# Kernel optimization log

Hardware: AMD Instinct MI355X
Metric: run time of the kernel (lower is better)

## Reference

```python
import jax, jax.numpy as jnp
import numpy as np

N = 50000
E = 800000
IN_C, HID_C, OUT_C = 256, 128, 64


def setup_inputs() -> dict:
    key = jax.random.key(0)
    k1, k2, k3, k4 = jax.random.split(key, 4)
    x = jax.random.normal(k1, (N, IN_C), dtype=jnp.float32)
    edge_index = jax.random.randint(k2, (2, E), 0, N, dtype=jnp.int64)
    # Glorot-ish init for GCN weights, zero bias (PyG default)
    W1 = jax.random.normal(k3, (IN_C, HID_C), dtype=jnp.float32) / np.sqrt(IN_C)
    b1 = jnp.zeros((HID_C,), dtype=jnp.float32)
    W2 = jax.random.normal(k4, (HID_C, OUT_C), dtype=jnp.float32) / np.sqrt(HID_C)
    b2 = jnp.zeros((OUT_C,), dtype=jnp.float32)
    return {"x": x, "edge_index": edge_index, "W1": W1, "b1": b1, "W2": W2, "b2": b2}


def _gcn_norm(edge_index, num_nodes):
    # Add self-loops, compute symmetric normalization D^-1/2 A D^-1/2 (PyG GCNConv default)
    loops = jnp.arange(num_nodes, dtype=edge_index.dtype)
    src = jnp.concatenate([edge_index[0], loops])  # message sources
    dst = jnp.concatenate([edge_index[1], loops])  # aggregation targets
    deg = jax.ops.segment_sum(jnp.ones_like(dst, dtype=jnp.float32), dst,
                              num_segments=num_nodes)
    dinv = jnp.where(deg > 0, jax.lax.rsqrt(deg), 0.0)
    norm = dinv[src] * dinv[dst]  # [E+N]
    return src, dst, norm


def _gcn_conv(x, W, b, src, dst, norm, num_nodes):
    h = x @ W                                   # [N, out]
    msg = h[src] * norm[:, None]                # gather + scale, [E+N, out]
    out = jax.ops.segment_sum(msg, dst, num_segments=num_nodes)  # scatter-add
    return out + b


def reference(x, edge_index, W1, b1, W2, b2):
    num_nodes = x.shape[0]
    src, dst, norm = _gcn_norm(edge_index, num_nodes)
    h = _gcn_conv(x, W1, b1, src, dst, norm, num_nodes)
    h = jax.nn.relu(h)
    # F.dropout(training=False) -> identity at inference
    return _gcn_conv(h, W2, b2, src, dst, norm, num_nodes)
```

## Files before the change

### kernel.cpp

```cpp
#include <hip/hip_runtime.h>
#include <hip/hip_bf16.h>


typedef __attribute__((ext_vector_type(8))) short short8;
typedef __attribute__((ext_vector_type(4))) float f32x4;

union BF8 {
    short8 s;
    uint4 u;
    __hip_bfloat162 h[4];
};

__device__ __forceinline__ unsigned short f32_to_bf16_rne(float f) {
    unsigned u = __float_as_uint(f);
    return (unsigned short)((u + 0x7fffu + ((u >> 16) & 1u)) >> 16);
}
__device__ __forceinline__ float bf_lo(unsigned v) { return __uint_as_float(v << 16); }
__device__ __forceinline__ float bf_hi(unsigned v) { return __uint_as_float(v & 0xffff0000u); }

#define ACHUNK 2048
#define BSH 6
#define BN 64
#define CAP 2048
#define EPT (CAP / 256)

__global__ void wfrag_zero_kernel(const float* __restrict__ W1, const float* __restrict__ W2,
                                  unsigned short* __restrict__ w1f,
                                  unsigned short* __restrict__ w2f,
                                  int* __restrict__ counts, int* __restrict__ bcursor,
                                  int n, int nbk) {
    int i = blockIdx.x * blockDim.x + threadIdx.x;
    if (i < n) counts[i] = 0;
    if (i < nbk) bcursor[i] = 0;
    const float* W;
    unsigned short* WF;
    int KS, NCOL, idx;
    if (i < 32768) {
        W = W1; WF = w1f; KS = 8; NCOL = 128; idx = i;
    } else if (i < 32768 + 8192) {
        W = W2; WF = w2f; KS = 4; NCOL = 64; idx = i - 32768;
    } else return;
    int j = idx & 7;
    int lane = (idx >> 3) & 63;
    int f = idx >> 9;
    int ks = f % KS, nt = f / KS;
    int m16 = lane & 15, quad = lane >> 4;
    int ncol = nt * 16 + m16;
    int k = ks * 32 + quad * 8 + j;
    WF[idx] = f32_to_bf16_rne(W[k * NCOL + ncol]);
}

__global__ __launch_bounds__(256, 8) void gemm1_bucket_kernel(
    const float* __restrict__ A, const unsigned short* __restrict__ BFRAG,
    unsigned short* __restrict__ C, int M, int nbA,
    const int* __restrict__ src, const int* __restrict__ dst,
    int* __restrict__ counts, int* __restrict__ bcursor,
    int2* __restrict__ tmp, int e, int nbk) {
    constexpr int NT = 8, KS = 8;
    constexpr int K = KS * 32;
    constexpr int LSTRIDE = 136;
    __shared__ unsigned short Alds[64 * LSTRIDE];

    const int tid = threadIdx.x;
    if ((int)blockIdx.x >= nbA) {
        const int wave = tid >> 6, lane = tid & 63;
        const int quad = lane >> 4, m16 = lane & 15;
        const int rowBase = (blockIdx.x - nbA) * 64;
        const uint4* Bfrag = (const uint4*)BFRAG + lane;

        f32x4 acc[NT];
#pragma unroll
        for (int nt = 0; nt < NT; nt++) acc[nt] = f32x4{0.f, 0.f, 0.f, 0.f};

#pragma unroll
        for (int h = 0; h < 2; h++) {
            if (h) __syncthreads();
#pragma unroll
            for (int bt = 0; bt < 2; bt++) {
                f32x4 v[4];
#pragma unroll
                for (int it = 0; it < 4; it++) {
                    int p = (bt * 4 + it) * 1024 + tid * 4;
                    int r = p >> 7, c = p & 127;
                    int rg = rowBase + r;
                    if (rg >= M) rg = M - 1;
                    v[it] = *(const f32x4*)(A + (size_t)rg * K + h * 128 + c);
                }
#pragma unroll
                for (int it = 0; it < 4; it++) {
                    int p = (bt * 4 + it) * 1024 + tid * 4;
                    int r = p >> 7, c = p & 127;
                    BF8 cv;
                    cv.h[0] = __float22bfloat162_rn(make_float2(v[it].x, v[it].y));
                    cv.h[1] = __float22bfloat162_rn(make_float2(v[it].z, v[it].w));
                    *(uint2*)&Alds[r * LSTRIDE + c] = make_uint2(cv.u.x, cv.u.y);
                }
            }
            __syncthreads();
            const unsigned short* Afrag0 = &Alds[(wave * 16 + m16) * LSTRIDE + quad * 8];
#pragma unroll
            for (int ks = 0; ks < 4; ks++) {
                BF8 af;
                af.u = *(const uint4*)(Afrag0 + ks * 32);
                int kg = h * 4 + ks;
#pragma unroll
                for (int nt = 0; nt < NT; nt++) {
                    BF8 bf;
                    bf.u = Bfrag[(nt * KS + kg) * 64];
                    acc[nt] = __builtin_amdgcn_mfma_f32_16x16x32_bf16(af.s, bf.s, acc[nt], 0, 0, 0);
                }
            }
        }
        const int rowOut = rowBase + wave * 16 + quad * 4;
#pragma unroll
        for (int nt = 0; nt < NT; nt++) {
#pragma unroll
            for (int r = 0; r < 4; r++) {
                int row = rowOut + r;
                if (row < M)
                    C[(size_t)row * 128 + nt * 16 + m16] = f32_to_bf16_rne(acc[nt][r]);
            }
        }
    } else {
        int* sdst = (int*)Alds;
        int* hist = (int*)((char*)Alds + ACHUNK * 4);
        const int b0 = blockIdx.x;
        const int start = b0 * ACHUNK;
        const int cnt = min(ACHUNK, e - start);
        for (int t = tid; t < nbk; t += 256) hist[t] = 0;
        __syncthreads();
        for (int i = tid; i < cnt; i += 256) {
            int d = dst[start + i];
            sdst[i] = d;
            atomicAdd(&counts[d], 1);
            atomicAdd(&hist[d >> BSH], 1);
        }
        __syncthreads();
        for (int t = tid; t < nbk; t += 256) {
            int h = hist[t];
            hist[t] = (h > 0) ? atomicAdd(&bcursor[t], h) : 0;
        }
        __syncthreads();
        for (int i = tid; i < cnt; i += 256) {
            int d = sdst[i];
            int slot = atomicAdd(&hist[d >> BSH], 1);
            if (slot < CAP)
                tmp[(size_t)(d >> BSH) * CAP + slot] = make_int2(src[start + i], d);
        }
    }
}

__global__ __launch_bounds__(256, 8) void aggsort_gemm2_kernel(
    const int* __restrict__ counts, const int2* __restrict__ tmp,
    const int* __restrict__ bcursor,
    const unsigned short* __restrict__ hb,
    const float* __restrict__ bias1,
    const unsigned short* __restrict__ w2frag,
    int2* __restrict__ sedge, int2* __restrict__ nodeRange,
    unsigned short* __restrict__ h2, int n) {
    constexpr int LSTRIDE = 136;
    __shared__ int ecnt[BN];
    __shared__ int estart[BN];
    __shared__ int lcur[BN];
    __shared__ float ndinv[BN];
    __shared__ unsigned short a1lds[BN * LSTRIDE];

    const int tid = threadIdx.x;
    const int b = blockIdx.x;
    const int nodeBase = b << BSH;
    const int nNodes = min(BN, n - nodeBase);
    const int cnt = min(bcursor[b], CAP);

    if (tid < BN) ecnt[tid] = 0;
    __syncthreads();

    int2 er[EPT];
#pragma unroll
    for (int j = 0; j < EPT; j++) {
        int i = tid + j * 256;
        if (i < cnt) {
            int2 r = tmp[(size_t)b * CAP + i];
            er[j] = r;
            atomicAdd(&ecnt[r.y - nodeBase], 1);
        } else {
            er[j].x = -1;
            er[j].y = 0;
        }
    }
    __syncthreads();

    if (tid < BN) {
        int c = ecnt[tid];
        int x = c;
#pragma unroll
        for (int off = 1; off < 64; off <<= 1) {
            int y = __shfl_up(x, off, 64);
            if (tid >= off) x += y;
        }
        int st = x - c;
        estart[tid] = st;
        lcur[tid] = st;
        ndinv[tid] = rsqrtf((float)c + 1.0f);
        if (tid < nNodes) nodeRange[nodeBase + tid] = make_int2(b * CAP + st, c);
    }
    __syncthreads();

#pragma unroll
    for (int j = 0; j < EPT; j++) {
        if (er[j].x >= 0) {
            int ln = er[j].y - nodeBase;
            float w = rsqrtf((float)counts[er[j].x] + 1.0f) * ndinv[ln];
            int pos = atomicAdd(&lcur[ln], 1);
            sedge[(size_t)b * CAP + pos] = make_int2(er[j].x, __float_as_int(w));
        }
    }
    __syncthreads();

    const int sub = tid & 15;
    const int qw = tid >> 4;
    for (int pass = 0; pass < BN / 16; pass++) {
        int ln = pass * 16 + qw;
        float a0 = 0.f, a1 = 0.f, a2 = 0.f, a3 = 0.f;
        float a4 = 0.f, a5 = 0.f, a6 = 0.f, a7 = 0.f;
        if (ln < nNodes) {
            int node = nodeBase + ln;
            float di = ndinv[ln];
            float d2 = di * di;
            uint4 sv = ((const uint4*)(hb + (size_t)node * 128))[sub];
            a0 = d2 * bf_lo(sv.x); a1 = d2 * bf_hi(sv.x);
            a2 = d2 * bf_lo(sv.y); a3 = d2 * bf_hi(sv.y);
            a4 = d2 * bf_lo(sv.z); a5 = d2 * bf_hi(sv.z);
            a6 = d2 * bf_lo(sv.w); a7 = d2 * bf_hi(sv.w);
            const int2* seg = sedge + (size_t)b * CAP;
            int beg = estart[ln];
            int end = beg + ecnt[ln];
            int i = beg;
            for (; i + 4 <= end; i += 4) {
                int2 e[4]; uint4 v[4];
#pragma unroll
                for (int j = 0; j < 4; j++) e[j] = seg[i + j];
#pragma unroll
                for (int j = 0; j < 4; j++)
                    v[j] = ((const uint4*)(hb + (size_t)e[j].x * 128))[sub];
#pragma unroll
                for (int j = 0; j < 4; j++) {
                    float w = __int_as_float(e[j].y);
                    a0 = fmaf(w, bf_lo(v[j].x), a0); a1 = fmaf(w, bf_hi(v[j].x), a1);
                    a2 = fmaf(w, bf_lo(v[j].y), a2); a3 = fmaf(w, bf_hi(v[j].y), a3);
                    a4 = fmaf(w, bf_lo(v[j].z), a4); a5 = fmaf(w, bf_hi(v[j].z), a5);
                    a6 = fmaf(w, bf_lo(v[j].w), a6); a7 = fmaf(w, bf_hi(v[j].w), a7);
                }
            }
            for (; i < end; ++i) {
                int2 e = seg[i];
                float w = __int_as_float(e.y);
                uint4 v = ((const uint4*)(hb + (size_t)e.x * 128))[sub];
                a0 = fmaf(w, bf_lo(v.x), a0); a1 = fmaf(w, bf_hi(v.x), a1);
                a2 = fmaf(w, bf_lo(v.y), a2); a3 = fmaf(w, bf_hi(v.y), a3);
                a4 = fmaf(w, bf_lo(v.z), a4); a5 = fmaf(w, bf_hi(v.z), a5);
                a6 = fmaf(w, bf_lo(v.w), a6); a7 = fmaf(w, bf_hi(v.w), a7);
            }
            float4 b0v = ((const float4*)bias1)[sub * 2];
            float4 b1v = ((const float4*)bias1)[sub * 2 + 1];
            a0 = fmaxf(a0 + b0v.x, 0.f); a1 = fmaxf(a1 + b0v.y, 0.f);
            a2 = fmaxf(a2 + b0v.z, 0.f); a3 = fmaxf(a3 + b0v.w, 0.f);
            a4 = fmaxf(a4 + b1v.x, 0.f); a5 = fmaxf(a5 + b1v.y, 0.f);
            a6 = fmaxf(a6 + b1v.z, 0.f); a7 = fmaxf(a7 + b1v.w, 0.f);
        }
        BF8 p;
        p.h[0] = __float22bfloat162_rn(make_float2(a0, a1));
        p.h[1] = __float22bfloat162_rn(make_float2(a2, a3));
        p.h[2] = __float22bfloat162_rn(make_float2(a4, a5));
        p.h[3] = __float22bfloat162_rn(make_float2(a6, a7));
        *(uint4*)&a1lds[ln * LSTRIDE + sub * 8] = p.u;
    }
    __syncthreads();

    const int wave = tid >> 6, lane = tid & 63;
    const int quad = lane >> 4, m16 = lane & 15;
    const unsigned short* Afrag0 = &a1lds[(wave * 16 + m16) * LSTRIDE + quad * 8];
    const uint4* Bfrag = (const uint4*)w2frag + lane;

    f32x4 acc[4];
#pragma unroll
    for (int nt = 0; nt < 4; nt++) acc[nt] = f32x4{0.f, 0.f, 0.f, 0.f};
#pragma unroll
    for (int ks = 0; ks < 4; ks++) {
        BF8 af;
        af.u = *(const uint4*)(Afrag0 + ks * 32);
#pragma unroll
        for (int nt = 0; nt < 4; nt++) {
            BF8 bf;
            bf.u = Bfrag[(nt * 4 + ks) * 64];
            acc[nt] = __builtin_amdgcn_mfma_f32_16x16x32_bf16(af.s, bf.s, acc[nt], 0, 0, 0);
        }
    }
    const int rowOut = wave * 16 + quad * 4;
#pragma unroll
    for (int nt = 0; nt < 4; nt++) {
#pragma unroll
        for (int r = 0; r < 4; r++) {
            int row = rowOut + r;
            if (row < nNodes)
                h2[(size_t)(nodeBase + row) * 64 + nt * 16 + m16] =
                    f32_to_bf16_rne(acc[nt][r]);
        }
    }
}

__global__ __launch_bounds__(256, 8) void agg64_kernel(
    const int2* __restrict__ nodeRange, const int2* __restrict__ sedge,
    const unsigned short* __restrict__ hb,
    const float* __restrict__ bias, float* __restrict__ out, int n) {
    int node = blockIdx.x * 16 + (threadIdx.x >> 4);
    if (node >= n) return;
    int sub = threadIdx.x & 15;
    int2 nr = nodeRange[node];
    float di = rsqrtf((float)nr.y + 1.0f);
    float d2 = di * di;
    uint2 sv = ((const uint2*)(hb + (size_t)node * 64))[sub];
    float a0 = d2 * bf_lo(sv.x), a1 = d2 * bf_hi(sv.x);
    float a2 = d2 * bf_lo(sv.y), a3 = d2 * bf_hi(sv.y);
    int beg = nr.x, end = nr.x + nr.y;
    int i = beg;
    for (; i + 8 <= end; i += 8) {
        int2 e[8];
        uint2 v[8];
#pragma unroll
        for (int j = 0; j < 8; j++) e[j] = sedge[i + j];
#pragma unroll
        for (int j = 0; j < 8; j++)
            v[j] = ((const uint2*)(hb + (size_t)e[j].x * 64))[sub];
#pragma unroll
        for (int j = 0; j < 8; j++) {
            float w = __int_as_float(e[j].y);
            a0 = fmaf(w, bf_lo(v[j].x), a0); a1 = fmaf(w, bf_hi(v[j].x), a1);
            a2 = fmaf(w, bf_lo(v[j].y), a2); a3 = fmaf(w, bf_hi(v[j].y), a3);
        }
    }
    for (; i + 4 <= end; i += 4) {
        int2 e[4];
        uint2 v[4];
#pragma unroll
        for (int j = 0; j < 4; j++) e[j] = sedge[i + j];
#pragma unroll
        for (int j = 0; j < 4; j++)
            v[j] = ((const uint2*)(hb + (size_t)e[j].x * 64))[sub];
#pragma unroll
        for (int j = 0; j < 4; j++) {
            float w = __int_as_float(e[j].y);
            a0 = fmaf(w, bf_lo(v[j].x), a0); a1 = fmaf(w, bf_hi(v[j].x), a1);
            a2 = fmaf(w, bf_lo(v[j].y), a2); a3 = fmaf(w, bf_hi(v[j].y), a3);
        }
    }
    for (; i < end; ++i) {
        int2 e = sedge[i];
        float w = __int_as_float(e.y);
        uint2 v = ((const uint2*)(hb + (size_t)e.x * 64))[sub];
        a0 = fmaf(w, bf_lo(v.x), a0); a1 = fmaf(w, bf_hi(v.x), a1);
        a2 = fmaf(w, bf_lo(v.y), a2); a3 = fmaf(w, bf_hi(v.y), a3);
    }
    float4 bv = ((const float4*)bias)[sub];
    ((float4*)(out + (size_t)node * 64))[sub] =
        make_float4(a0 + bv.x, a1 + bv.y, a2 + bv.z, a3 + bv.w);
}

extern "C" void kernel_launch(void* const* d_in, const int* in_sizes, int n_in,
                              void* d_out, int out_size, void* d_ws, size_t ws_size,
                              hipStream_t stream) {
    const float* x  = (const float*)d_in[0];
    const int*   ei = (const int*)d_in[1];
    const float* W1 = (const float*)d_in[2];
    const float* b1 = (const float*)d_in[3];
    const float* W2 = (const float*)d_in[4];
    const float* b2 = (const float*)d_in[5];
    float* out = (float*)d_out;

    const int IN_C = 256;
    const int N = in_sizes[0] / IN_C;
    const int E = in_sizes[1] / 2;
    const int* srcA = ei;
    const int* dstA = ei + E;

    char* ws = (char*)d_ws;
    const size_t KB = 1024, MB = 1024 * 1024;
    int*            counts    = (int*)(ws);
    int*            bcursor   = (int*)(ws + 256 * KB);
    unsigned short* w1f       = (unsigned short*)(ws + 1 * MB);
    unsigned short* w2f       = (unsigned short*)(ws + 1 * MB + 64 * KB);
    int2*           tmp       = (int2*)(ws + 2 * MB);
    int2*           sedge     = (int2*)(ws + 16 * MB);
    int2*           nodeRange = (int2*)(ws + 30 * MB);
    unsigned short* h1b       = (unsigned short*)(ws + 31 * MB);
    unsigned short* h2b       = (unsigned short*)(ws + 44 * MB);

    const int NB = (N + BN - 1) / BN;
    const int gGemm = (N + 63) / 64;
    const int nbA = (E + ACHUNK - 1) / ACHUNK;
    const int gWfrag = (max(N, 32768 + 8192) + 255) / 256;

    wfrag_zero_kernel<<<gWfrag, 256, 0, stream>>>(W1, W2, w1f, w2f, counts, bcursor, N, NB);
    gemm1_bucket_kernel<<<nbA + gGemm, 256, 0, stream>>>(
        x, w1f, h1b, N, nbA, srcA, dstA, counts, bcursor, tmp, E, NB);
    aggsort_gemm2_kernel<<<NB, 256, 0, stream>>>(
        counts, tmp, bcursor, h1b, b1, w2f, sedge, nodeRange, h2b, N);
    agg64_kernel<<<(N + 15) / 16, 256, 0, stream>>>(nodeRange, sedge, h2b, b2, out, N);
}
```

Measured before the change: 242.6 us.

## Replace multi-kernel pipeline with single cooperative persistent kernel using grid syncs

Merges the four launches into one cooperative kernel that uses grid-wide barriers between phases: weight fragment conversion, degree counting, a decoupled-lookback prefix scan fused with GEMM1 tiles, a CSR build through global atomic scatter, then a fused layer-1 aggregation plus GEMM2, and the final aggregation. It drops the bucketed tmp/CAP scheme in favour of an exact rowptr CSR, and shrinks GEMM tiles to 16 rows. The aim is to cut launch gaps and intermediate traffic. In exchange it adds several grid syncs, heavy global atomics on rowptr, serialized lookback spinning, and lower occupancy from the larger persistent kernel.

```diff
diff --git a/kernel.cpp b/kernel.cpp
--- a/kernel.cpp
+++ b/kernel.cpp
@@ -1,5 +1,8 @@
 #include <hip/hip_runtime.h>
 #include <hip/hip_bf16.h>
+#include <hip/hip_cooperative_groups.h>
+
+namespace cg = cooperative_groups;
 
 
 typedef __attribute__((ext_vector_type(8))) short short8;
@@ -18,351 +21,303 @@
 __device__ __forceinline__ float bf_lo(unsigned v) { return __uint_as_float(v << 16); }
 __device__ __forceinline__ float bf_hi(unsigned v) { return __uint_as_float(v & 0xffff0000u); }
 
-#define ACHUNK 2048
-#define BSH 6
-#define BN 64
-#define CAP 2048
-#define EPT (CAP / 256)
-
-__global__ void wfrag_zero_kernel(const float* __restrict__ W1, const float* __restrict__ W2,
-                                  unsigned short* __restrict__ w1f,
-                                  unsigned short* __restrict__ w2f,
-                                  int* __restrict__ counts, int* __restrict__ bcursor,
-                                  int n, int nbk) {
-    int i = blockIdx.x * blockDim.x + threadIdx.x;
-    if (i < n) counts[i] = 0;
-    if (i < nbk) bcursor[i] = 0;
-    const float* W;
-    unsigned short* WF;
-    int KS, NCOL, idx;
-    if (i < 32768) {
-        W = W1; WF = w1f; KS = 8; NCOL = 128; idx = i;
-    } else if (i < 32768 + 8192) {
-        W = W2; WF = w2f; KS = 4; NCOL = 64; idx = i - 32768;
-    } else return;
-    int j = idx & 7;
-    int lane = (idx >> 3) & 63;
-    int f = idx >> 9;
-    int ks = f % KS, nt = f / KS;
-    int m16 = lane & 15, quad = lane >> 4;
-    int ncol = nt * 16 + m16;
-    int k = ks * 32 + quad * 8 + j;
-    WF[idx] = f32_to_bf16_rne(W[k * NCOL + ncol]);
-}
-
-__global__ __launch_bounds__(256, 8) void gemm1_bucket_kernel(
-    const float* __restrict__ A, const unsigned short* __restrict__ BFRAG,
-    unsigned short* __restrict__ C, int M, int nbA,
-    const int* __restrict__ src, const int* __restrict__ dst,
-    int* __restrict__ counts, int* __restrict__ bcursor,
-    int2* __restrict__ tmp, int e, int nbk) {
-    constexpr int NT = 8, KS = 8;
-    constexpr int K = KS * 32;
-    constexpr int LSTRIDE = 136;
-    __shared__ unsigned short Alds[64 * LSTRIDE];
-
+__global__ __launch_bounds__(256) void mega_kernel(
+    const float* __restrict__ x, const int* __restrict__ srcA, const int* __restrict__ dstA,
+    const float* __restrict__ W1, const float* __restrict__ b1,
+    const float* __restrict__ W2, const float* __restrict__ b2,
+    float* __restrict__ out,
+    int* __restrict__ counts, float* __restrict__ dinv, int* __restrict__ rowptr,
+    int* __restrict__ bflag, int* __restrict__ bsum,
+    unsigned short* __restrict__ w1f, unsigned short* __restrict__ w2f,
+    int2* __restrict__ sedge, unsigned short* __restrict__ h1b,
+    unsigned short* __restrict__ h2b,
+    int n, int e, int nScan, int nG1, int nAgg) {
+    cg::grid_group gg = cg::this_grid();
     const int tid = threadIdx.x;
-    if ((int)blockIdx.x >= nbA) {
-        const int wave = tid >> 6, lane = tid & 63;
-        const int quad = lane >> 4, m16 = lane & 15;
-        const int rowBase = (blockIdx.x - nbA) * 64;
-        const uint4* Bfrag = (const uint4*)BFRAG + lane;
-
-        f32x4 acc[NT];
-#pragma unroll
-        for (int nt = 0; nt < NT; nt++) acc[nt] = f32x4{0.f, 0.f, 0.f, 0.f};
-
-#pragma unroll
-        for (int h = 0; h < 2; h++) {
-            if (h) __syncthreads();
-#pragma unroll
-            for (int bt = 0; bt < 2; bt++) {
-                f32x4 v[4];
-#pragma unroll
-                for (int it = 0; it < 4; it++) {
-                    int p = (bt * 4 + it) * 1024 + tid * 4;
-                    int r = p >> 7, c = p & 127;
-                    int rg = rowBase + r;
-                    if (rg >= M) rg = M - 1;
-                    v[it] = *(const f32x4*)(A + (size_t)rg * K + h * 128 + c);
-                }
-#pragma unroll
-                for (int it = 0; it < 4; it++) {
-                    int p = (bt * 4 + it) * 1024 + tid * 4;
-                    int r = p >> 7, c = p & 127;
-                    BF8 cv;
-                    cv.h[0] = __float22bfloat162_rn(make_float2(v[it].x, v[it].y));
-                    cv.h[1] = __float22bfloat162_rn(make_float2(v[it].z, v[it].w));
-                    *(uint2*)&Alds[r * LSTRIDE + c] = make_uint2(cv.u.x, cv.u.y);
-                }
-            }
+    const int bid = blockIdx.x;
+    const int nblk = gridDim.x;
+    const int gstride = nblk * 256;
+    __shared__ char smraw[16 * 136 * 2 + 32];
+
+    {
+        int lim = n > 40960 ? n : 40960;
+        for (int i = bid * 256 + tid; i < lim; i += gstride) {
+            if (i < n) counts[i] = 0;
+            if (i < 64) bflag[i] = 0;
+            if (i < 40960) {
+                const float* W; unsigned short* WF; int KS, NCOL, idx;
+                if (i < 32768) { W = W1; WF = w1f; KS = 8; NCOL = 128; idx = i; }
+                else           { W = W2; WF = w2f; KS = 4; NCOL = 64;  idx = i - 32768; }
+                int j = idx & 7;
+                int lane = (idx >> 3) & 63;
+                int f = idx >> 9;
+                int ks = f % KS, nt = f / KS;
+                int m16 = lane & 15, quad = lane >> 4;
+                WF[idx] = f32_to_bf16_rne(W[(ks * 32 + quad * 8 + j) * NCOL + nt * 16 + m16]);
+            }
+        }
+    }
+    gg.sync();
+
+    for (int i = bid * 256 + tid; i < e; i += gstride)
+        atomicAdd(&counts[dstA[i]], 1);
+    gg.sync();
+
+    for (int it = bid; it < nScan + nG1; it += nblk) {
+        if (it < nScan) {
+            int* wsum = (int*)(smraw + 16 * 136 * 2);
+            const int lane = tid & 63, wv = tid >> 6;
+            int base = it * 1024 + tid * 4;
+            int v[4];
+#pragma unroll
+            for (int j = 0; j < 4; j++) {
+                int i = base + j;
+                if (i < n) {
+                    int c = counts[i];
+                    v[j] = c;
+                    dinv[i] = rsqrtf((float)c + 1.0f);
+                } else v[j] = 0;
+            }
+            int tot = v[0] + v[1] + v[2] + v[3];
+            int xp = tot;
+#pragma unroll
+            for (int off = 1; off < 64; off <<= 1) {
+                int y = __shfl_up(xp, off, 64);
+                if (lane >= off) xp += y;
+            }
+            if (lane == 63) wsum[wv] = xp;
             __syncthreads();
-            const unsigned short* Afrag0 = &Alds[(wave * 16 + m16) * LSTRIDE + quad * 8];
-#pragma unroll
-            for (int ks = 0; ks < 4; ks++) {
-                BF8 af;
-                af.u = *(const uint4*)(Afrag0 + ks * 32);
-                int kg = h * 4 + ks;
-#pragma unroll
-                for (int nt = 0; nt < NT; nt++) {
-                    BF8 bf;
-                    bf.u = Bfrag[(nt * KS + kg) * 64];
-                    acc[nt] = __builtin_amdgcn_mfma_f32_16x16x32_bf16(af.s, bf.s, acc[nt], 0, 0, 0);
+            int wpre = 0;
+            for (int k = 0; k < wv; k++) wpre += wsum[k];
+            if (tid == 0) {
+                bsum[it] = wsum[0] + wsum[1] + wsum[2] + wsum[3];
+                __threadfence();
+                atomicExch(&bflag[it], 1);
+            }
+            if (wv == 0) {
+                int p = 0;
+                if (lane < it) {
+                    while (atomicAdd(&bflag[lane], 0) == 0) {}
+                    __threadfence();
+                    p = atomicAdd(&bsum[lane], 0);
+                }
+#pragma unroll
+                for (int off = 1; off < 64; off <<= 1) p += __shfl_xor(p, off, 64);
+                if (lane == 0) wsum[4] = p;
+            }
+            __syncthreads();
+            int pre = wsum[4] + wpre + (xp - tot);
+#pragma unroll
+            for (int j = 0; j < 4; j++) {
+                int i = base + j;
+                if (i <= n) rowptr[i] = pre;
+                pre += v[j];
+            }
+        } else {
+            const int t16 = it - nScan;
+            unsigned short* Alds = (unsigned short*)smraw;
+            const int wave = tid >> 6, lane = tid & 63;
+            const int quad = lane >> 4, m16 = lane & 15;
+            const int rowBase = t16 * 16;
+            f32x4 acc[2];
+            acc[0] = f32x4{0.f, 0.f, 0.f, 0.f};
+            acc[1] = f32x4{0.f, 0.f, 0.f, 0.f};
+#pragma unroll
+            for (int h = 0; h < 2; h++) {
+                __syncthreads();
+                int p0 = tid * 4, p1 = 1024 + tid * 4;
+                int r0 = p0 >> 7, c0 = p0 & 127;
+                int r1 = p1 >> 7, c1 = p1 & 127;
+                int rg0 = rowBase + r0; if (rg0 >= n) rg0 = n - 1;
+                int rg1 = rowBase + r1; if (rg1 >= n) rg1 = n - 1;
+                f32x4 v0 = *(const f32x4*)(x + (size_t)rg0 * 256 + h * 128 + c0);
+                f32x4 v1 = *(const f32x4*)(x + (size_t)rg1 * 256 + h * 128 + c1);
+                BF8 cv;
+                cv.h[0] = __float22bfloat162_rn(make_float2(v0.x, v0.y));
+                cv.h[1] = __float22bfloat162_rn(make_float2(v0.z, v0.w));
+                *(uint2*)&Alds[r0 * 136 + c0] = make_uint2(cv.u.x, cv.u.y);
+                cv.h[0] = __float22bfloat162_rn(make_float2(v1.x, v1.y));
+                cv.h[1] = __float22bfloat162_rn(make_float2(v1.z, v1.w));
+                *(uint2*)&Alds[r1 * 136 + c1] = make_uint2(cv.u.x, cv.u.y);
+                __syncthreads();
+                const unsigned short* Af0 = &Alds[m16 * 136 + quad * 8];
+#pragma unroll
+                for (int ks = 0; ks < 4; ks++) {
+                    BF8 af;
+                    af.u = *(const uint4*)(Af0 + ks * 32);
+                    int kg = h * 4 + ks;
+#pragma unroll
+                    for (int nt = 0; nt < 2; nt++) {
+                        BF8 bf;
+                        bf.u = ((const uint4*)w1f)[((wave * 2 + nt) * 8 + kg) * 64 + lane];
+                        acc[nt] = __builtin_amdgcn_mfma_f32_16x16x32_bf16(af.s, bf.s, acc[nt], 0, 0, 0);
+                    }
+                }
+            }
+            const int rowOut = rowBase + quad * 4;
+#pragma unroll
+            for (int nt = 0; nt < 2; nt++) {
+#pragma unroll
+                for (int r = 0; r < 4; r++) {
+                    int row = rowOut + r;
+                    if (row < n)
+                        h1b[(size_t)row * 128 + (wave * 2 + nt) * 16 + m16] =
+                            f32_to_bf16_rne(acc[nt][r]);
                 }
             }
         }
-        const int rowOut = rowBase + wave * 16 + quad * 4;
-#pragma unroll
-        for (int nt = 0; nt < NT; nt++) {
-#pragma unroll
-            for (int r = 0; r < 4; r++) {
-                int row = rowOut + r;
-                if (row < M)
-                    C[(size_t)row * 128 + nt * 16 + m16] = f32_to_bf16_rne(acc[nt][r]);
-            }
+    }
+    gg.sync();
+
+    for (int i = bid * 256 + tid; i < e; i += gstride) {
+        int s = srcA[i], d = dstA[i];
+        float w = dinv[s] * dinv[d];
+        int pos = atomicAdd(&rowptr[d], 1);
+        sedge[pos] = make_int2(s, __float_as_int(w));
+    }
+    gg.sync();
+
+    {
+        unsigned short* a1lds = (unsigned short*)smraw;
+        const int sub = tid & 15, qw = tid >> 4;
+        for (int it = bid; it < nAgg; it += nblk) {
+            int node = it * 16 + qw;
+            float a0 = 0.f, a1 = 0.f, a2 = 0.f, a3 = 0.f;
+            float a4 = 0.f, a5 = 0.f, a6 = 0.f, a7 = 0.f;
+            if (node < n) {
+                float di = dinv[node], d2 = di * di;
+                uint4 sv = ((const uint4*)(h1b + (size_t)node * 128))[sub];
+                a0 = d2 * bf_lo(sv.x); a1 = d2 * bf_hi(sv.x);
+                a2 = d2 * bf_lo(sv.y); a3 = d2 * bf_hi(sv.y);
+                a4 = d2 * bf_lo(sv.z); a5 = d2 * bf_hi(sv.z);
+                a6 = d2 * bf_lo(sv.w); a7 = d2 * bf_hi(sv.w);
+                int beg = (node > 0) ? rowptr[node - 1] : 0;
+                int end = rowptr[node];
+                int i = beg;
+                for (; i + 4 <= end; i += 4) {
+                    int2 ed[4]; uint4 v[4];
+#pragma unroll
+                    for (int j = 0; j < 4; j++) ed[j] = sedge[i + j];
+#pragma unroll
+                    for (int j = 0; j < 4; j++)
+                        v[j] = ((const uint4*)(h1b + (size_t)ed[j].x * 128))[sub];
+#pragma unroll
+                    for (int j = 0; j < 4; j++) {
+                        float w = __int_as_float(ed[j].y);
+                        a0 = fmaf(w, bf_lo(v[j].x), a0); a1 = fmaf(w, bf_hi(v[j].x), a1);
+                        a2 = fmaf(w, bf_lo(v[j].y), a2); a3 = fmaf(w, bf_hi(v[j].y), a3);
+                        a4 = fmaf(w, bf_lo(v[j].z), a4); a5 = fmaf(w, bf_hi(v[j].z), a5);
+                        a6 = fmaf(w, bf_lo(v[j].w), a6); a7 = fmaf(w, bf_hi(v[j].w), a7);
+                    }
+                }
+                for (; i < end; ++i) {
+                    int2 ed = sedge[i];
+                    float w = __int_as_float(ed.y);
+                    uint4 v = ((const uint4*)(h1b + (size_t)ed.x * 128))[sub];
+                    a0 = fmaf(w, bf_lo(v.x), a0); a1 = fmaf(w, bf_hi(v.x), a1);
+                    a2 = fmaf(w, bf_lo(v.y), a2); a3 = fmaf(w, bf_hi(v.y), a3);
+                    a4 = fmaf(w, bf_lo(v.z), a4); a5 = fmaf(w, bf_hi(v.z), a5);
+                    a6 = fmaf(w, bf_lo(v.w), a6); a7 = fmaf(w, bf_hi(v.w), a7);
+                }
+                float4 b0v = ((const float4*)b1)[sub * 2];
+                float4 b1v = ((const float4*)b1)[sub * 2 + 1];
+                a0 = fmaxf(a0 + b0v.x, 0.f); a1 = fmaxf(a1 + b0v.y, 0.f);
+                a2 = fmaxf(a2 + b0v.z, 0.f); a3 = fmaxf(a3 + b0v.w, 0.f);
+                a4 = fmaxf(a4 + b1v.x, 0.f); a5 = fmaxf(a5 + b1v.y, 0.f);
+                a6 = fmaxf(a6 + b1v.z, 0.f); a7 = fmaxf(a7 + b1v.w, 0.f);
+            }
+            BF8 p;
+            p.h[0] = __float22bfloat162_rn(make_float2(a0, a1));
+            p.h[1] = __float22bfloat162_rn(make_float2(a2, a3));
+            p.h[2] = __float22bfloat162_rn(make_float2(a4, a5));
+            p.h[3] = __float22bfloat162_rn(make_float2(a6, a7));
+            *(uint4*)&a1lds[qw * 136 + sub * 8] = p.u;
+            __syncthreads();
+            if (tid < 64) {
+                const int quad = tid >> 4, m16 = tid & 15;
+                const unsigned short* Af0 = &a1lds[m16 * 136 + quad * 8];
+                f32x4 acc2[4];
+#pragma unroll
+                for (int nt = 0; nt < 4; nt++) acc2[nt] = f32x4{0.f, 0.f, 0.f, 0.f};
+#pragma unroll
+                for (int ks = 0; ks < 4; ks++) {
+                    BF8 af;
+                    af.u = *(const uint4*)(Af0 + ks * 32);
+#pragma unroll
+                    for (int nt = 0; nt < 4; nt++) {
+                        BF8 bf;
+                        bf.u = ((const uint4*)w2f)[(nt * 4 + ks) * 64 + tid];
+                        acc2[nt] = __builtin_amdgcn_mfma_f32_16x16x32_bf16(af.s, bf.s, acc2[nt], 0, 0, 0);
+                    }
+                }
+                const int rowOut = it * 16 + quad * 4;
+#pragma unroll
+                for (int nt = 0; nt < 4; nt++) {
+#pragma unroll
+                    for (int r = 0; r < 4; r++) {
+                        int row = rowOut + r;
+                        if (row < n)
+                            h2b[(size_t)row * 64 + nt * 16 + m16] = f32_to_bf16_rne(acc2[nt][r]);
+                    }
+                }
+            }
+            __syncthreads();
         }
-    } else {
-        int* sdst = (int*)Alds;
-        int* hist = (int*)((char*)Alds + ACHUNK * 4);
-        const int b0 = blockIdx.x;
-        const int start = b0 * ACHUNK;
-        const int cnt = min(ACHUNK, e - start);
-        for (int t = tid; t < nbk; t += 256) hist[t] = 0;
-        __syncthreads();
-        for (int i = tid; i < cnt; i += 256) {
-            int d = dst[start + i];
-            sdst[i] = d;
-            atomicAdd(&counts[d], 1);
-            atomicAdd(&hist[d >> BSH], 1);
-        }
-        __syncthreads();
-        for (int t = tid; t < nbk; t += 256) {
-            int h = hist[t];
-            hist[t] = (h > 0) ? atomicAdd(&bcursor[t], h) : 0;
-        }
-        __syncthreads();
-        for (int i = tid; i < cnt; i += 256) {
-            int d = sdst[i];
-            int slot = atomicAdd(&hist[d >> BSH], 1);
-            if (slot < CAP)
-                tmp[(size_t)(d >> BSH) * CAP + slot] = make_int2(src[start + i], d);
-        }
-    }
-}
-
-__global__ __launch_bounds__(256, 8) void aggsort_gemm2_kernel(
-    const int* __restrict__ counts, const int2* __restrict__ tmp,
-    const int* __restrict__ bcursor,
-    const unsigned short* __restrict__ hb,
-    const float* __restrict__ bias1,
-    const unsigned short* __restrict__ w2frag,
-    int2* __restrict__ sedge, int2* __restrict__ nodeRange,
-    unsigned short* __restrict__ h2, int n) {
-    constexpr int LSTRIDE = 136;
-    __shared__ int ecnt[BN];
-    __shared__ int estart[BN];
-    __shared__ int lcur[BN];
-    __shared__ float ndinv[BN];
-    __shared__ unsigned short a1lds[BN * LSTRIDE];
-
-    const int tid = threadIdx.x;
-    const int b = blockIdx.x;
-    const int nodeBase = b << BSH;
-    const int nNodes = min(BN, n - nodeBase);
-    const int cnt = min(bcursor[b], CAP);
-
-    if (tid < BN) ecnt[tid] = 0;
-    __syncthreads();
-
-    int2 er[EPT];
-#pragma unroll
-    for (int j = 0; j < EPT; j++) {
-        int i = tid + j * 256;
-        if (i < cnt) {
-            int2 r = tmp[(size_t)b * CAP + i];
-            er[j] = r;
-            atomicAdd(&ecnt[r.y - nodeBase], 1);
-        } else {
-            er[j].x = -1;
-            er[j].y = 0;
-        }
-    }
-    __syncthreads();
-
-    if (tid < BN) {
-        int c = ecnt[tid];
-        int x = c;
-#pragma unroll
-        for (int off = 1; off < 64; off <<= 1) {
-            int y = __shfl_up(x, off, 64);
-            if (tid >= off) x += y;
-        }
-        int st = x - c;
-        estart[tid] = st;
-        lcur[tid] = st;
-        ndinv[tid] = rsqrtf((float)c + 1.0f);
-        if (tid < nNodes) nodeRange[nodeBase + tid] = make_int2(b * CAP + st, c);
-    }
-    __syncthreads();
-
-#pragma unroll
-    for (int j = 0; j < EPT; j++) {
-        if (er[j].x >= 0) {
-            int ln = er[j].y - nodeBase;
-            float w = rsqrtf((float)counts[er[j].x] + 1.0f) * ndinv[ln];
-            int pos = atomicAdd(&lcur[ln], 1);
-            sedge[(size_t)b * CAP + pos] = make_int2(er[j].x, __float_as_int(w));
-        }
-    }
-    __syncthreads();
-
-    const int sub = tid & 15;
-    const int qw = tid >> 4;
-    for (int pass = 0; pass < BN / 16; pass++) {
-        int ln = pass * 16 + qw;
-        float a0 = 0.f, a1 = 0.f, a2 = 0.f, a3 = 0.f;
-        float a4 = 0.f, a5 = 0.f, a6 = 0.f, a7 = 0.f;
-        if (ln < nNodes) {
-            int node = nodeBase + ln;
-            float di = ndinv[ln];
-            float d2 = di * di;
-            uint4 sv = ((const uint4*)(hb + (size_t)node * 128))[sub];
-            a0 = d2 * bf_lo(sv.x); a1 = d2 * bf_hi(sv.x);
-            a2 = d2 * bf_lo(sv.y); a3 = d2 * bf_hi(sv.y);
-            a4 = d2 * bf_lo(sv.z); a5 = d2 * bf_hi(sv.z);
-            a6 = d2 * bf_lo(sv.w); a7 = d2 * bf_hi(sv.w);
-            const int2* seg = sedge + (size_t)b * CAP;
-            int beg = estart[ln];
-            int end = beg + ecnt[ln];
+    }
+    gg.sync();
+
+    {
+        const int sub = tid & 15, qw = tid >> 4;
+        for (int it = bid; it < nAgg; it += nblk) {
+            int node = it * 16 + qw;
+            if (node >= n) continue;
+            float di = dinv[node], d2 = di * di;
+            uint2 sv = ((const uint2*)(h2b + (size_t)node * 64))[sub];
+            float a0 = d2 * bf_lo(sv.x), a1 = d2 * bf_hi(sv.x);
+            float a2 = d2 * bf_lo(sv.y), a3 = d2 * bf_hi(sv.y);
+            int beg = (node > 0) ? rowptr[node - 1] : 0;
+            int end = rowptr[node];
             int i = beg;
-            for (; i + 4 <= end; i += 4) {
-                int2 e[4]; uint4 v[4];
-#pragma unroll
-                for (int j = 0; j < 4; j++) e[j] = seg[i + j];
-#pragma unroll
-                for (int j = 0; j < 4; j++)
-                    v[j] = ((const uint4*)(hb + (size_t)e[j].x * 128))[sub];
-#pragma unroll
-                for (int j = 0; j < 4; j++) {
-                    float w = __int_as_float(e[j].y);
+            for (; i + 8 <= end; i += 8) {
+                int2 ed[8]; uint2 v[8];
+#pragma unroll
+                for (int j = 0; j < 8; j++) ed[j] = sedge[i + j];
+#pragma unroll
+                for (int j = 0; j < 8; j++)
+                    v[j] = ((const uint2*)(h2b + (size_t)ed[j].x * 64))[sub];
+#pragma unroll
+                for (int j = 0; j < 8; j++) {
+                    float w = __int_as_float(ed[j].y);
                     a0 = fmaf(w, bf_lo(v[j].x), a0); a1 = fmaf(w, bf_hi(v[j].x), a1);
                     a2 = fmaf(w, bf_lo(v[j].y), a2); a3 = fmaf(w, bf_hi(v[j].y), a3);
-                    a4 = fmaf(w, bf_lo(v[j].z), a4); a5 = fmaf(w, bf_hi(v[j].z), a5);
-                    a6 = fmaf(w, bf_lo(v[j].w), a6); a7 = fmaf(w, bf_hi(v[j].w), a7);
+                }
+            }
+            for (; i + 4 <= end; i += 4) {
+                int2 ed[4]; uint2 v[4];
+#pragma unroll
+                for (int j = 0; j < 4; j++) ed[j] = sedge[i + j];
+#pragma unroll
+                for (int j = 0; j < 4; j++)
+                    v[j] = ((const uint2*)(h2b + (size_t)ed[j].x * 64))[sub];
+#pragma unroll
+                for (int j = 0; j < 4; j++) {
+                    float w = __int_as_float(ed[j].y);
+                    a0 = fmaf(w, bf_lo(v[j].x), a0); a1 = fmaf(w, bf_hi(v[j].x), a1);
+                    a2 = fmaf(w, bf_lo(v[j].y), a2); a3 = fmaf(w, bf_hi(v[j].y), a3);
                 }
             }
             for (; i < end; ++i) {
-                int2 e = seg[i];
-                float w = __int_as_float(e.y);
-                uint4 v = ((const uint4*)(hb + (size_t)e.x * 128))[sub];
+                int2 ed = sedge[i];
+                float w = __int_as_float(ed.y);
+                uint2 v = ((const uint2*)(h2b + (size_t)ed.x * 64))[sub];
                 a0 = fmaf(w, bf_lo(v.x), a0); a1 = fmaf(w, bf_hi(v.x), a1);
                 a2 = fmaf(w, bf_lo(v.y), a2); a3 = fmaf(w, bf_hi(v.y), a3);
-                a4 = fmaf(w, bf_lo(v.z), a4); a5 = fmaf(w, bf_hi(v.z), a5);
-                a6 = fmaf(w, bf_lo(v.w), a6); a7 = fmaf(w, bf_hi(v.w), a7);
-            }
-            float4 b0v = ((const float4*)bias1)[sub * 2];
-            float4 b1v = ((const float4*)bias1)[sub * 2 + 1];
-            a0 = fmaxf(a0 + b0v.x, 0.f); a1 = fmaxf(a1 + b0v.y, 0.f);
-            a2 = fmaxf(a2 + b0v.z, 0.f); a3 = fmaxf(a3 + b0v.w, 0.f);
-            a4 = fmaxf(a4 + b1v.x, 0.f); a5 = fmaxf(a5 + b1v.y, 0.f);
-            a6 = fmaxf(a6 + b1v.z, 0.f); a7 = fmaxf(a7 + b1v.w, 0.f);
+            }
+            float4 bv = ((const float4*)b2)[sub];
+            ((float4*)(out + (size_t)node * 64))[sub] =
+                make_float4(a0 + bv.x, a1 + bv.y, a2 + bv.z, a3 + bv.w);
         }
-        BF8 p;
-        p.h[0] = __float22bfloat162_rn(make_float2(a0, a1));
-        p.h[1] = __float22bfloat162_rn(make_float2(a2, a3));
-        p.h[2] = __float22bfloat162_rn(make_float2(a4, a5));
-        p.h[3] = __float22bfloat162_rn(make_float2(a6, a7));
-        *(uint4*)&a1lds[ln * LSTRIDE + sub * 8] = p.u;
-    }
-    __syncthreads();
-
-    const int wave = tid >> 6, lane = tid & 63;
-    const int quad = lane >> 4, m16 = lane & 15;
-    const unsigned short* Afrag0 = &a1lds[(wave * 16 + m16) * LSTRIDE + quad * 8];
-    const uint4* Bfrag = (const uint4*)w2frag + lane;
-
-    f32x4 acc[4];
-#pragma unroll
-    for (int nt = 0; nt < 4; nt++) acc[nt] = f32x4{0.f, 0.f, 0.f, 0.f};
-#pragma unroll
-    for (int ks = 0; ks < 4; ks++) {
-        BF8 af;
-        af.u = *(const uint4*)(Afrag0 + ks * 32);
-#pragma unroll
-        for (int nt = 0; nt < 4; nt++) {
-            BF8 bf;
-            bf.u = Bfrag[(nt * 4 + ks) * 64];
-            acc[nt] = __builtin_amdgcn_mfma_f32_16x16x32_bf16(af.s, bf.s, acc[nt], 0, 0, 0);
-        }
-    }
-    const int rowOut = wave * 16 + quad * 4;
-#pragma unroll
-    for (int nt = 0; nt < 4; nt++) {
-#pragma unroll
-        for (int r = 0; r < 4; r++) {
-            int row = rowOut + r;
-            if (row < nNodes)
-                h2[(size_t)(nodeBase + row) * 64 + nt * 16 + m16] =
-                    f32_to_bf16_rne(acc[nt][r]);
-        }
-    }
-}
-
-__global__ __launch_bounds__(256, 8) void agg64_kernel(
-    const int2* __restrict__ nodeRange, const int2* __restrict__ sedge,
-    const unsigned short* __restrict__ hb,
-    const float* __restrict__ bias, float* __restrict__ out, int n) {
-    int node = blockIdx.x * 16 + (threadIdx.x >> 4);
-    if (node >= n) return;
-    int sub = threadIdx.x & 15;
-    int2 nr = nodeRange[node];
-    float di = rsqrtf((float)nr.y + 1.0f);
-    float d2 = di * di;
-    uint2 sv = ((const uint2*)(hb + (size_t)node * 64))[sub];
-    float a0 = d2 * bf_lo(sv.x), a1 = d2 * bf_hi(sv.x);
-    float a2 = d2 * bf_lo(sv.y), a3 = d2 * bf_hi(sv.y);
-    int beg = nr.x, end = nr.x + nr.y;
-    int i = beg;
-    for (; i + 8 <= end; i += 8) {
-        int2 e[8];
-        uint2 v[8];
-#pragma unroll
-        for (int j = 0; j < 8; j++) e[j] = sedge[i + j];
-#pragma unroll
-        for (int j = 0; j < 8; j++)
-            v[j] = ((const uint2*)(hb + (size_t)e[j].x * 64))[sub];
-#pragma unroll
-        for (int j = 0; j < 8; j++) {
-            float w = __int_as_float(e[j].y);
-            a0 = fmaf(w, bf_lo(v[j].x), a0); a1 = fmaf(w, bf_hi(v[j].x), a1);
-            a2 = fmaf(w, bf_lo(v[j].y), a2); a3 = fmaf(w, bf_hi(v[j].y), a3);
-        }
-    }
-    for (; i + 4 <= end; i += 4) {
-        int2 e[4];
-        uint2 v[4];
-#pragma unroll
-        for (int j = 0; j < 4; j++) e[j] = sedge[i + j];
-#pragma unroll
-        for (int j = 0; j < 4; j++)
-            v[j] = ((const uint2*)(hb + (size_t)e[j].x * 64))[sub];
-#pragma unroll
-        for (int j = 0; j < 4; j++) {
-            float w = __int_as_float(e[j].y);
-            a0 = fmaf(w, bf_lo(v[j].x), a0); a1 = fmaf(w, bf_hi(v[j].x), a1);
-            a2 = fmaf(w, bf_lo(v[j].y), a2); a3 = fmaf(w, bf_hi(v[j].y), a3);
-        }
-    }
-    for (; i < end; ++i) {
-        int2 e = sedge[i];
-        float w = __int_as_float(e.y);
-        uint2 v = ((const uint2*)(hb + (size_t)e.x * 64))[sub];
-        a0 = fmaf(w, bf_lo(v.x), a0); a1 = fmaf(w, bf_hi(v.x), a1);
-        a2 = fmaf(w, bf_lo(v.y), a2); a3 = fmaf(w, bf_hi(v.y), a3);
-    }
-    float4 bv = ((const float4*)bias)[sub];
-    ((float4*)(out + (size_t)node * 64))[sub] =
-        make_float4(a0 + bv.x, a1 + bv.y, a2 + bv.z, a3 + bv.w);
+    }
 }
 
 extern "C" void kernel_launch(void* const* d_in, const int* in_sizes, int n_in,
@@ -377,32 +332,45 @@
     float* out = (float*)d_out;
 
     const int IN_C = 256;
-    const int N = in_sizes[0] / IN_C;
-    const int E = in_sizes[1] / 2;
+    int N = in_sizes[0] / IN_C;
+    int E = in_sizes[1] / 2;
     const int* srcA = ei;
     const int* dstA = ei + E;
 
     char* ws = (char*)d_ws;
     const size_t KB = 1024, MB = 1024 * 1024;
-    int*            counts    = (int*)(ws);
-    int*            bcursor   = (int*)(ws + 256 * KB);
-    unsigned short* w1f       = (unsigned short*)(ws + 1 * MB);
-    unsigned short* w2f       = (unsigned short*)(ws + 1 * MB + 64 * KB);
-    int2*           tmp       = (int2*)(ws + 2 * MB);
-    int2*           sedge     = (int2*)(ws + 16 * MB);
-    int2*           nodeRange = (int2*)(ws + 30 * MB);
-    unsigned short* h1b       = (unsigned short*)(ws + 31 * MB);
-    unsigned short* h2b       = (unsigned short*)(ws + 44 * MB);
-
-    const int NB = (N + BN - 1) / BN;
-    const int gGemm = (N + 63) / 64;
-    const int nbA = (E + ACHUNK - 1) / ACHUNK;
-    const int gWfrag = (max(N, 32768 + 8192) + 255) / 256;
-
-    wfrag_zero_kernel<<<gWfrag, 256, 0, stream>>>(W1, W2, w1f, w2f, counts, bcursor, N, NB);
-    gemm1_bucket_kernel<<<nbA + gGemm, 256, 0, stream>>>(
-        x, w1f, h1b, N, nbA, srcA, dstA, counts, bcursor, tmp, E, NB);
-    aggsort_gemm2_kernel<<<NB, 256, 0, stream>>>(
-        counts, tmp, bcursor, h1b, b1, w2f, sedge, nodeRange, h2b, N);
-    agg64_kernel<<<(N + 15) / 16, 256, 0, stream>>>(nodeRange, sedge, h2b, b2, out, N);
+    int*            counts = (int*)(ws);
+    float*          dinv   = (float*)(ws + 256 * KB);
+    int*            rowptr = (int*)(ws + 512 * KB);
+    int*            bflag  = (int*)(ws + 768 * KB);
+    int*            bsum   = (int*)(ws + 772 * KB);
+    unsigned short* w1f    = (unsigned short*)(ws + 1 * MB);
+    unsigned short* w2f    = (unsigned short*)(ws + 1 * MB + 64 * KB);
+    int2*           sedge  = (int2*)(ws + 2 * MB);
+    unsigned short* h1b    = (unsigned short*)(ws + 9 * MB);
+    unsigned short* h2b    = (unsigned short*)(ws + 22 * MB);
+
+    int nScan = (N + 1 + 1023) / 1024;
+    int nG1   = (N + 15) / 16;
+    int nAgg  = (N + 15) / 16;
+
+    static int gridBlocks = 0;
+    if (gridBlocks == 0) {
+        int occ = 0;
+        hipOccupancyMaxActiveBlocksPerMultiprocessor(&occ, mega_kernel, 256, 0);
+        if (occ < 1) occ = 1;
+        int dev = 0, nCU = 0;
+        hipGetDevice(&dev);
+        hipDeviceGetAttribute(&nCU, hipDeviceAttributeMultiprocessorCount, dev);
+        if (nCU <= 0) nCU = 256;
+        gridBlocks = occ * nCU;
+    }
+
+    void* args[] = {(void*)&x, (void*)&srcA, (void*)&dstA, (void*)&W1, (void*)&b1,
+                    (void*)&W2, (void*)&b2, (void*)&out,
+                    (void*)&counts, (void*)&dinv, (void*)&rowptr, (void*)&bflag, (void*)&bsum,
+                    (void*)&w1f, (void*)&w2f, (void*)&sedge, (void*)&h1b, (void*)&h2b,
+                    (void*)&N, (void*)&E, (void*)&nScan, (void*)&nG1, (void*)&nAgg};
+    hipLaunchCooperativeKernel((const void*)mega_kernel, dim3(gridBlocks), dim3(256),
+                               args, 0, stream);
 }
```

After: 505.7 us. +108.5%, slower.
